# Kernel tuning notes

Measured on AMD Instinct MI355X. Metric: run time of the kernel, lower is better.

Reference implementation:

```python
import jax, jax.numpy as jnp
import numpy as np

NUM_HEADS = 8
SIGMA = 1.0
LAMBDA_INIT = 0.1
GAMMA_INIT = 0.001


def _pos_encoding(H, W, d_model):
    # 2D sinusoidal encoding: first half encodes x (width), second half y (height)
    d = d_model // 2
    div = jnp.exp(jnp.arange(0, d, 2, dtype=jnp.float32) * (-np.log(10000.0) / d))
    xs = jnp.arange(W, dtype=jnp.float32)[:, None] * div  # (W, d//2)
    ys = jnp.arange(H, dtype=jnp.float32)[:, None] * div  # (H, d//2)
    pe_x = jnp.stack([jnp.sin(xs), jnp.cos(xs)], axis=-1).reshape(W, d)
    pe_y = jnp.stack([jnp.sin(ys), jnp.cos(ys)], axis=-1).reshape(H, d)
    pe = jnp.concatenate([
        jnp.broadcast_to(pe_x[None, :, :], (H, W, d)),
        jnp.broadcast_to(pe_y[:, None, :], (H, W, d)),
    ], axis=-1)
    return pe  # (H, W, d_model)


def _distance_map(H, W, sigma):
    # exp(-euclidean_dist / sigma) between all flattened pixel positions
    yy, xx = jnp.meshgrid(jnp.arange(H, dtype=jnp.float32), jnp.arange(W, dtype=jnp.float32), indexing='ij')
    coords = jnp.stack([yy.reshape(-1), xx.reshape(-1)], axis=-1)  # (HW, 2)
    d2 = jnp.sum((coords[:, None, :] - coords[None, :, :]) ** 2, axis=-1)
    return jnp.exp(-jnp.sqrt(d2) / sigma)  # (HW, HW)


def _conv1x1(x, w, b):
    # 1x1 conv == channel matmul; x: (B,C,H,W), w: (O,C), b: (O,)
    return jnp.einsum('bchw,oc->bohw', x, w) + b[None, :, None, None]


def setup_inputs() -> dict:
    key = jax.random.key(0)
    ks = jax.random.split(key, 9)
    B, C, H, W = 2, 256, 48, 48
    d_model = 256
    inp = {
        'x': jax.random.normal(ks[0], (B, C, H, W), dtype=jnp.float32),
        'Wq': jax.random.normal(ks[1], (d_model, C), dtype=jnp.float32) * 0.01,
        'bq': jnp.zeros((d_model,), dtype=jnp.float32),
        'Wk': jax.random.normal(ks[2], (d_model, C), dtype=jnp.float32) * 0.01,
        'bk': jnp.zeros((d_model,), dtype=jnp.float32),
        'Wv': jax.random.normal(ks[3], (d_model, C), dtype=jnp.float32) * 0.01,
        'bv': jnp.zeros((d_model,), dtype=jnp.float32),
        'Wo': jax.random.normal(ks[4], (C, d_model), dtype=jnp.float32) * 0.01,
        'bo': jnp.zeros((C,), dtype=jnp.float32),
        'lambda_dist': jnp.float32(LAMBDA_INIT),
        'gamma': jnp.float32(GAMMA_INIT),
    }
    return inp


def reference(x, Wq, bq, Wk, bk, Wv, bv, Wo, bo, lambda_dist, gamma):
    B, C, H, W = x.shape
    d_model = Wq.shape[0]
    d_k = d_model // NUM_HEADS
    pe = _pos_encoding(H, W, d_model).transpose(2, 0, 1)[None]  # (1, d_model, H, W)
    dm = _distance_map(H, W, SIGMA)                              # (HW, HW)

    q = _conv1x1(x, Wq, bq) + pe
    k = _conv1x1(x, Wk, bk) + pe
    v = _conv1x1(x, Wv, bv)

    def heads(t):
        return t.reshape(B, NUM_HEADS, d_k, H * W).transpose(0, 1, 3, 2)  # (B,h,HW,d_k)

    Q, K, V = heads(q), heads(k), heads(v)
    scores = jnp.einsum('bhnd,bhmd->bhnm', Q, K) / jnp.sqrt(jnp.float32(d_k))
    scores = scores + (lambda_dist * dm)[None, None]  # 'exp' distance prior bias
    attn = jax.nn.softmax(scores, axis=-1)
    out = jnp.einsum('bhnm,bhmd->bhnd', attn, V)
    out = out.transpose(0, 1, 3, 2).reshape(B, d_model, H, W)
    fused = gamma * out  # simple weighted fusion, single (self) branch
    return x + _conv1x1(fused, Wo, bo)
```

## Files before the change

### kernel.cpp

```cpp
#include <hip/hip_runtime.h>

#define HW 2304
#define SW 48
#define DMODEL 256
#define NHEADS 8
#define DK 32
#define BATCH 2

typedef unsigned short u16;
typedef __attribute__((ext_vector_type(8))) short short8;
typedef __attribute__((ext_vector_type(4))) float f32x4;

__device__ __forceinline__ float bf2f(u16 v) {
  union { unsigned int u; float f; } c; c.u = ((unsigned int)v) << 16; return c.f;
}
__device__ __forceinline__ float lo2f(unsigned int u) {
  union { unsigned int u; float f; } c; c.u = u << 16; return c.f;
}
__device__ __forceinline__ float hi2f(unsigned int u) {
  union { unsigned int u; float f; } c; c.u = u & 0xffff0000u; return c.f;
}
__device__ __forceinline__ u16 f2bf(float f) {
  union { unsigned int u; float f; } c; c.f = f;
  unsigned int u = c.u;
  unsigned int r = (u + 0x7FFFu + ((u >> 16) & 1u)) >> 16;
  return (u16)r;
}
__device__ __forceinline__ int div48(int n) { return (n * 87382) >> 22; }
__device__ __forceinline__ int swz(int row, int k) {
  return ((row >> 4) << 12) + ((k >> 3) << 7) + ((row & 15) << 3) + (k & 7);
}

__global__ __launch_bounds__(256) void prep_kernel(
    const float* __restrict__ x,
    const float* __restrict__ Wq, const float* __restrict__ Wk,
    const float* __restrict__ Wv, const float* __restrict__ Wo,
    const float* __restrict__ lam_p,
    u16* __restrict__ xt, u16* __restrict__ Wb, u16* __restrict__ et) {
  int bid = blockIdx.x;
  int t = threadIdx.x;
  if (bid < 288) {
    int b = bid / 144, r = bid % 144;
    int c0 = (r / 36) * 64, n0 = (r % 36) * 64;
    __shared__ u16 sh[64][72];
#pragma unroll
    for (int p = 0; p < 4; ++p) {
      int row = (t >> 4) + p * 16;
      int col4 = (t & 15) * 4;
      float4 v = *(const float4*)(x + (size_t)(b * DMODEL + c0 + row) * HW +
                                  n0 + col4);
      sh[col4 + 0][row] = f2bf(v.x);
      sh[col4 + 1][row] = f2bf(v.y);
      sh[col4 + 2][row] = f2bf(v.z);
      sh[col4 + 3][row] = f2bf(v.w);
    }
    __syncthreads();
    u16* xtb = xt + (size_t)b * HW * DMODEL;
#pragma unroll
    for (int q = 0; q < 2; ++q) {
      int nrow = t >> 2;
      int c8 = (t & 3) * 8 + q * 32;
      *(uint4*)(xtb + swz(n0 + nrow, c0 + c8)) = *(const uint4*)&sh[nrow][c8];
    }
  } else if (bid < 544) {
    int idx = (bid - 288) * 1024 + t * 4;
    int which = idx >> 16, off = idx & 65535;
    int m = off >> 8, k = off & 255;
    const float* src = (which == 0) ? Wq : (which == 1) ? Wk
                       : (which == 2) ? Wv : Wo;
    float4 v = *(const float4*)(src + off);
    ushort4 ov;
    ov.x = f2bf(v.x); ov.y = f2bf(v.y); ov.z = f2bf(v.z); ov.w = f2bf(v.w);
    *(ushort4*)(Wb + which * 65536 + swz(m, k)) = ov;
  } else {
    int id = (bid - 544) * 256 + t;
    int flat = id * 8;
    int tile = flat >> 8;
    int within = flat & 255;
    int tm = tile / 144, tq = tile - tm * 144;
    int m = tm * 16 + (within >> 4);
    int q = tq * 16 + (within & 15);
    int ym = div48(m), xm = m - ym * SW;
    int yq = div48(q), xq = q - yq * SW;
    float lam = lam_p[0];
    float dy = (float)(yq - ym);
    float dy2 = dy * dy;
    u16 o[8];
#pragma unroll
    for (int j = 0; j < 8; ++j) {
      float dx = (float)(xq + j - xm);
      o[j] = f2bf(lam * __expf(-sqrtf(dy2 + dx * dx)));
    }
    *(uint4*)(et + flat) = *(const uint4*)o;
  }
}

__global__ __launch_bounds__(256) void qkv_kernel(
    const u16* __restrict__ Wb, const u16* __restrict__ xt,
    const float* __restrict__ bq, const float* __restrict__ bk,
    const float* __restrict__ bv,
    u16* __restrict__ qt, u16* __restrict__ ktb, u16* __restrict__ vb) {
  int t = threadIdx.x;
  int w = t >> 6, lane = t & 63, lo = lane & 15, quad = lane >> 4;
  int n0 = blockIdx.x * 64;
  int mb = blockIdx.y, b = blockIdx.z;
  int which = mb >> 2;
  int mrel0 = (mb & 3) * 64;
  const u16* A = Wb + which * 65536 + ((mrel0 + w * 16) >> 4) * 4096 + lo * 8;
  const float* bias = (which == 0) ? bq : (which == 1) ? bk : bv;
  const u16* Bx = xt + (size_t)b * HW * DMODEL + lo * 8;

  f32x4 acc[4] = {{0.f, 0.f, 0.f, 0.f}, {0.f, 0.f, 0.f, 0.f},
                  {0.f, 0.f, 0.f, 0.f}, {0.f, 0.f, 0.f, 0.f}};
#pragma unroll
  for (int k0 = 0; k0 < DMODEL; k0 += 32) {
    int kblk = ((k0 >> 3) + quad) << 7;
    short8 af = *(const short8*)(A + kblk);
#pragma unroll
    for (int nt = 0; nt < 4; ++nt) {
      short8 bf_ = *(const short8*)(Bx + ((n0 + nt * 16) >> 4) * 4096 + kblk);
      acc[nt] = __builtin_amdgcn_mfma_f32_16x16x32_bf16(af, bf_, acc[nt], 0, 0, 0);
    }
  }

  int mbase = mrel0 + w * 16 + quad * 4;
  if (which == 2) {
#pragma unroll
    for (int reg = 0; reg < 4; ++reg) {
      int mrel = mbase + reg;
      float bi = bias[mrel];
      u16* dst = vb + (size_t)(b * DMODEL + mrel) * HW + n0 + lo;
#pragma unroll
      for (int nt = 0; nt < 4; ++nt) dst[nt * 16] = f2bf(acc[nt][reg] + bi);
    }
  } else {
    float sc = (which == 0) ? 0.17677669529663687f : 1.0f;
    int h = mbase >> 5, d0 = mbase & 31;
    u16* base = ((which == 0) ? qt : ktb) + (size_t)(b * NHEADS + h) * HW * DK;
    float bi[4], dv[4];
    bool usecos[4], usey[4];
#pragma unroll
    for (int reg = 0; reg < 4; ++reg) {
      int mrel = mbase + reg;
      bi[reg] = bias[mrel];
      int oo = mrel & 127;
      dv[reg] = expf(-0.07195578415606394f * (float)(oo & ~1));
      usecos[reg] = (oo & 1);
      usey[reg] = (mrel >= 128);
    }
#pragma unroll
    for (int nt = 0; nt < 4; ++nt) {
      int n = n0 + nt * 16 + lo;
      int yy = div48(n), xx = n - yy * SW;
      ushort4 ov;
      float vals[4];
#pragma unroll
      for (int reg = 0; reg < 4; ++reg) {
        float tv = (usey[reg] ? (float)yy : (float)xx) * dv[reg];
        float pe = usecos[reg] ? cosf(tv) : sinf(tv);
        vals[reg] = (acc[nt][reg] + bi[reg] + pe) * sc;
      }
      ov.x = f2bf(vals[0]); ov.y = f2bf(vals[1]);
      ov.z = f2bf(vals[2]); ov.w = f2bf(vals[3]);
      *(ushort4*)(base + (size_t)n * DK + d0) = ov;
    }
  }
}

__global__ __launch_bounds__(256) void attn_kernel(
    const u16* __restrict__ qt, const u16* __restrict__ ktb,
    const u16* __restrict__ vb, const u16* __restrict__ et,
    u16* __restrict__ po_o, float* __restrict__ po_l) {
  int t = threadIdx.x;
  int w = t >> 6;
  int lane = t & 63;
  int lo = lane & 15, quad = lane >> 4;
  int n0 = blockIdx.x * 64;
  int h = blockIdx.y >> 2, kh = blockIdx.y & 3;
  int b = blockIdx.z;

  __shared__ u16 Ks[64 * 40];
  __shared__ u16 Vs[32 * 72];
  __shared__ u16 Ps[4 * 16 * 72];

  const u16* qtg = qt + (size_t)(b * NHEADS + h) * HW * DK;
  const u16* ktg = ktb + (size_t)(b * NHEADS + h) * HW * DK;
  const u16* vbg = vb + (size_t)(b * DMODEL + h * DK) * HW;

  short8 qf = *(const short8*)(qtg + (size_t)(n0 + w * 16 + lo) * DK + quad * 8);

  int tq = (n0 >> 4) + w;
  const u16* etw = et + (size_t)tq * 256 + lo * 16 + quad * 4;

  f32x4 o0 = {0.f, 0.f, 0.f, 0.f}, o1 = {0.f, 0.f, 0.f, 0.f};
  float lsum[4] = {0.f, 0.f, 0.f, 0.f};
  u16* psw = Ps + w * 16 * 72;

  for (int kt = kh * 9; kt < kh * 9 + 9; ++kt) {
    int m0 = kt * 64;
    __syncthreads();
    {
      int row = t >> 2, c8 = (t & 3) * 8;
      *(uint4*)&Ks[row * 40 + c8] =
          *(const uint4*)(ktg + (size_t)(m0 + row) * DK + c8);
      int dd = t >> 3, mo = (t & 7) * 8;
      *(uint4*)&Vs[dd * 72 + mo] =
          *(const uint4*)(vbg + (size_t)dd * HW + m0 + mo);
    }
    __syncthreads();

    uint2 ebv[4];
#pragma unroll
    for (int t4 = 0; t4 < 4; ++t4)
      ebv[t4] = *(const uint2*)(etw + (size_t)((m0 >> 4) + t4) * 36864);

    f32x4 s[4];
#pragma unroll
    for (int t4 = 0; t4 < 4; ++t4) {
      short8 kf = *(const short8*)&Ks[(t4 * 16 + lo) * 40 + quad * 8];
      f32x4 z = {0.f, 0.f, 0.f, 0.f};
      s[t4] = __builtin_amdgcn_mfma_f32_16x16x32_bf16(qf, kf, z, 0, 0, 0);
    }
#pragma unroll
    for (int t4 = 0; t4 < 4; ++t4) {
      float p0 = __expf(s[t4][0] + lo2f(ebv[t4].x));
      float p1 = __expf(s[t4][1] + hi2f(ebv[t4].x));
      float p2 = __expf(s[t4][2] + lo2f(ebv[t4].y));
      float p3 = __expf(s[t4][3] + hi2f(ebv[t4].y));
      lsum[0] += p0; lsum[1] += p1; lsum[2] += p2; lsum[3] += p3;
      psw[(quad * 4 + 0) * 72 + t4 * 16 + lo] = f2bf(p0);
      psw[(quad * 4 + 1) * 72 + t4 * 16 + lo] = f2bf(p1);
      psw[(quad * 4 + 2) * 72 + t4 * 16 + lo] = f2bf(p2);
      psw[(quad * 4 + 3) * 72 + t4 * 16 + lo] = f2bf(p3);
    }
#pragma unroll
    for (int ks = 0; ks < 2; ++ks) {
      short8 af = *(const short8*)&psw[lo * 72 + ks * 32 + quad * 8];
      short8 v0 = *(const short8*)&Vs[lo * 72 + ks * 32 + quad * 8];
      o0 = __builtin_amdgcn_mfma_f32_16x16x32_bf16(af, v0, o0, 0, 0, 0);
      short8 v1 = *(const short8*)&Vs[(16 + lo) * 72 + ks * 32 + quad * 8];
      o1 = __builtin_amdgcn_mfma_f32_16x16x32_bf16(af, v1, o1, 0, 0, 0);
    }
  }

#pragma unroll
  for (int d = 1; d < 16; d <<= 1) {
#pragma unroll
    for (int reg = 0; reg < 4; ++reg) lsum[reg] += __shfl_xor(lsum[reg], d);
  }

  int slot = (b * NHEADS + h) * 36 + blockIdx.x;
  u16* pw = po_o + (size_t)(kh * 576 + slot) * 2048 + w * 512;
  ushort4 s0, s1;
  s0.x = f2bf(o0[0]); s0.y = f2bf(o0[1]); s0.z = f2bf(o0[2]); s0.w = f2bf(o0[3]);
  s1.x = f2bf(o1[0]); s1.y = f2bf(o1[1]); s1.z = f2bf(o1[2]); s1.w = f2bf(o1[3]);
  *(ushort4*)(pw + lane * 4) = s0;
  *(ushort4*)(pw + 256 + lane * 4) = s1;
  if (lo == 0) {
    float4 lv = make_float4(lsum[0], lsum[1], lsum[2], lsum[3]);
    *(float4*)(po_l + (size_t)(kh * 576 + slot) * 64 + w * 16 + quad * 4) = lv;
  }
}

__global__ __launch_bounds__(256) void reduce_kernel(
    const u16* __restrict__ po_o, const float* __restrict__ po_l,
    u16* __restrict__ aot) {
  int t = threadIdx.x;
  int w = t >> 6, lane = t & 63, lo = lane & 15, quad = lane >> 4;
  int qt_ = blockIdx.x, h = blockIdx.y, b = blockIdx.z;
  int slot = (b * NHEADS + h) * 36 + qt_;

  float s0[4] = {0.f, 0.f, 0.f, 0.f}, s1[4] = {0.f, 0.f, 0.f, 0.f};
  float lt[4] = {0.f, 0.f, 0.f, 0.f};
#pragma unroll
  for (int kh = 0; kh < 4; ++kh) {
    const u16* p = po_o + (size_t)(kh * 576 + slot) * 2048 + w * 512;
    ushort4 a0 = *(const ushort4*)(p + lane * 4);
    ushort4 a1 = *(const ushort4*)(p + 256 + lane * 4);
    s0[0] += bf2f(a0.x); s0[1] += bf2f(a0.y);
    s0[2] += bf2f(a0.z); s0[3] += bf2f(a0.w);
    s1[0] += bf2f(a1.x); s1[1] += bf2f(a1.y);
    s1[2] += bf2f(a1.z); s1[3] += bf2f(a1.w);
    float4 lv = *(const float4*)(po_l + (size_t)(kh * 576 + slot) * 64 +
                                 w * 16 + quad * 4);
    lt[0] += lv.x; lt[1] += lv.y; lt[2] += lv.z; lt[3] += lv.w;
  }

  u16* aog = aot + (size_t)b * HW * DMODEL;
#pragma unroll
  for (int reg = 0; reg < 4; ++reg) {
    float inv = 1.0f / lt[reg];
    int n = qt_ * 64 + w * 16 + quad * 4 + reg;
    aog[swz(n, h * DK + lo)] = f2bf(s0[reg] * inv);
    aog[swz(n, h * DK + 16 + lo)] = f2bf(s1[reg] * inv);
  }
}

__global__ __launch_bounds__(256) void out_kernel(
    const float* __restrict__ x, const u16* __restrict__ Wob,
    const float* __restrict__ bo, const float* __restrict__ gp,
    const u16* __restrict__ aot, float* __restrict__ out) {
  int t = threadIdx.x;
  int w = t >> 6, lane = t & 63, lo = lane & 15, quad = lane >> 4;
  int n0 = blockIdx.x * 64;
  int c0 = blockIdx.y * 64;
  int b = blockIdx.z;
  float gamma = gp[0];
  const u16* A = Wob + ((c0 + w * 16) >> 4) * 4096 + lo * 8;
  const u16* Ba = aot + (size_t)b * HW * DMODEL + lo * 8;

  f32x4 acc[4] = {{0.f, 0.f, 0.f, 0.f}, {0.f, 0.f, 0.f, 0.f},
                  {0.f, 0.f, 0.f, 0.f}, {0.f, 0.f, 0.f, 0.f}};
#pragma unroll
  for (int k0 = 0; k0 < DMODEL; k0 += 32) {
    int kblk = ((k0 >> 3) + quad) << 7;
    short8 af = *(const short8*)(A + kblk);
#pragma unroll
    for (int nt = 0; nt < 4; ++nt) {
      short8 bf_ = *(const short8*)(Ba + ((n0 + nt * 16) >> 4) * 4096 + kblk);
      acc[nt] = __builtin_amdgcn_mfma_f32_16x16x32_bf16(af, bf_, acc[nt], 0, 0, 0);
    }
  }

#pragma unroll
  for (int reg = 0; reg < 4; ++reg) {
    int c = c0 + w * 16 + quad * 4 + reg;
    float bi = bo[c];
    const float* xs = x + (size_t)(b * DMODEL + c) * HW + n0 + lo;
    float* os = out + (size_t)(b * DMODEL + c) * HW + n0 + lo;
#pragma unroll
    for (int nt = 0; nt < 4; ++nt)
      os[nt * 16] = xs[nt * 16] + gamma * acc[nt][reg] + bi;
  }
}

extern "C" void kernel_launch(void* const* d_in, const int* in_sizes, int n_in,
                              void* d_out, int out_size, void* d_ws,
                              size_t ws_size, hipStream_t stream) {
  const float* x   = (const float*)d_in[0];
  const float* Wq  = (const float*)d_in[1];
  const float* bq  = (const float*)d_in[2];
  const float* Wk  = (const float*)d_in[3];
  const float* bk  = (const float*)d_in[4];
  const float* Wv  = (const float*)d_in[5];
  const float* bv  = (const float*)d_in[6];
  const float* Wo  = (const float*)d_in[7];
  const float* bo  = (const float*)d_in[8];
  const float* lam = (const float*)d_in[9];
  const float* gam = (const float*)d_in[10];

  char* wsb = (char*)d_ws;
  u16* Wb  = (u16*)(wsb + 36864);
  u16* xt  = (u16*)(wsb + 561152);
  u16* aot = xt;
  u16* qt  = (u16*)(wsb + 2920448);
  u16* ktb = (u16*)(wsb + 5279744);
  u16* vb  = (u16*)(wsb + 7639040);
  u16* et  = (u16*)(wsb + 9998336);
  u16* po_o = (u16*)(wsb + 20615168);
  float* po_l = (float*)(wsb + 30052352);
  float* out = (float*)d_out;

  prep_kernel<<<dim3(3136), 256, 0, stream>>>(x, Wq, Wk, Wv, Wo, lam,
                                              xt, Wb, et);
  qkv_kernel<<<dim3(36, 12, BATCH), 256, 0, stream>>>(Wb, xt, bq, bk, bv,
                                                      qt, ktb, vb);
  attn_kernel<<<dim3(36, 32, BATCH), 256, 0, stream>>>(qt, ktb, vb, et,
                                                       po_o, po_l);
  reduce_kernel<<<dim3(36, 8, BATCH), 256, 0, stream>>>(po_o, po_l, aot);
  out_kernel<<<dim3(36, 4, BATCH), 256, 0, stream>>>(x, Wb + 3 * 65536, bo, gam,
                                                     aot, out);
}
```

Baseline: 136.9 us.

## Compute transposed scores so P stays in registers, removing LDS round-trip

The attention kernel now computes S^T = K·Q^T with K rows permuted at load time, so each lane's MFMA output maps directly onto the B-operand fragment of the P·V MFMA. This removes the per-tile shared-memory buffer for P, its scattered 16-bit stores and reloads, and the per-row shuffle reduction of the row sums. The bias table must use a matching, differently tiled layout, and the output and row-sum layouts change, so the reduce kernel is updated to match. It relies on the prep code having produced the new bias layout; if it has not, results will be wrong.

```diff
diff --git a/kernel.cpp b/kernel.cpp
--- a/kernel.cpp
+++ b/kernel.cpp
@@ -181,7 +181,6 @@
 
   __shared__ u16 Ks[64 * 40];
   __shared__ u16 Vs[32 * 72];
-  __shared__ u16 Ps[4 * 16 * 72];
 
   const u16* qtg = qt + (size_t)(b * NHEADS + h) * HW * DK;
   const u16* ktg = ktb + (size_t)(b * NHEADS + h) * HW * DK;
@@ -189,65 +188,64 @@
 
   short8 qf = *(const short8*)(qtg + (size_t)(n0 + w * 16 + lo) * DK + quad * 8);
 
+  int srow = t >> 2;
+  int sks = srow >> 5, srr = srow & 31;
+  int sv = (srr < 16) ? (8 * (srr >> 2) + (srr & 3))
+                      : (8 * ((srr - 16) >> 2) + 4 + ((srr - 16) & 3));
+  int skey = sks * 32 + sv;
+  int sc8 = (t & 3) * 8;
+
   int tq = (n0 >> 4) + w;
-  const u16* etw = et + (size_t)tq * 256 + lo * 16 + quad * 4;
+  const u16* etw = et + (size_t)tq * 144 * 256 + lo * 16 + (quad & 1) * 8;
+  int qh = quad >> 1;
 
   f32x4 o0 = {0.f, 0.f, 0.f, 0.f}, o1 = {0.f, 0.f, 0.f, 0.f};
-  float lsum[4] = {0.f, 0.f, 0.f, 0.f};
-  u16* psw = Ps + w * 16 * 72;
+  float lsum = 0.f;
 
   for (int kt = kh * 9; kt < kh * 9 + 9; ++kt) {
     int m0 = kt * 64;
     __syncthreads();
     {
-      int row = t >> 2, c8 = (t & 3) * 8;
-      *(uint4*)&Ks[row * 40 + c8] =
-          *(const uint4*)(ktg + (size_t)(m0 + row) * DK + c8);
+      *(uint4*)&Ks[srow * 40 + sc8] =
+          *(const uint4*)(ktg + (size_t)(m0 + skey) * DK + sc8);
       int dd = t >> 3, mo = (t & 7) * 8;
       *(uint4*)&Vs[dd * 72 + mo] =
           *(const uint4*)(vbg + (size_t)dd * HW + m0 + mo);
     }
     __syncthreads();
 
-    uint2 ebv[4];
-#pragma unroll
-    for (int t4 = 0; t4 < 4; ++t4)
-      ebv[t4] = *(const uint2*)(etw + (size_t)((m0 >> 4) + t4) * 36864);
-
-    f32x4 s[4];
-#pragma unroll
-    for (int t4 = 0; t4 < 4; ++t4) {
-      short8 kf = *(const short8*)&Ks[(t4 * 16 + lo) * 40 + quad * 8];
+    uint4 eb0 = *(const uint4*)(etw + (size_t)((m0 >> 4) + 0 + qh) * 256);
+    uint4 eb1 = *(const uint4*)(etw + (size_t)((m0 >> 4) + 2 + qh) * 256);
+
+#pragma unroll
+    for (int ks = 0; ks < 2; ++ks) {
+      uint4 ebv = ks ? eb1 : eb0;
+      short8 kfA = *(const short8*)&Ks[(ks * 32 + lo) * 40 + quad * 8];
+      short8 kfB = *(const short8*)&Ks[(ks * 32 + 16 + lo) * 40 + quad * 8];
       f32x4 z = {0.f, 0.f, 0.f, 0.f};
-      s[t4] = __builtin_amdgcn_mfma_f32_16x16x32_bf16(qf, kf, z, 0, 0, 0);
-    }
-#pragma unroll
-    for (int t4 = 0; t4 < 4; ++t4) {
-      float p0 = __expf(s[t4][0] + lo2f(ebv[t4].x));
-      float p1 = __expf(s[t4][1] + hi2f(ebv[t4].x));
-      float p2 = __expf(s[t4][2] + lo2f(ebv[t4].y));
-      float p3 = __expf(s[t4][3] + hi2f(ebv[t4].y));
-      lsum[0] += p0; lsum[1] += p1; lsum[2] += p2; lsum[3] += p3;
-      psw[(quad * 4 + 0) * 72 + t4 * 16 + lo] = f2bf(p0);
-      psw[(quad * 4 + 1) * 72 + t4 * 16 + lo] = f2bf(p1);
-      psw[(quad * 4 + 2) * 72 + t4 * 16 + lo] = f2bf(p2);
-      psw[(quad * 4 + 3) * 72 + t4 * 16 + lo] = f2bf(p3);
-    }
-#pragma unroll
-    for (int ks = 0; ks < 2; ++ks) {
-      short8 af = *(const short8*)&psw[lo * 72 + ks * 32 + quad * 8];
+      f32x4 sA = __builtin_amdgcn_mfma_f32_16x16x32_bf16(kfA, qf, z, 0, 0, 0);
+      f32x4 sB = __builtin_amdgcn_mfma_f32_16x16x32_bf16(kfB, qf, z, 0, 0, 0);
+      float p0 = __expf(sA[0] + lo2f(ebv.x));
+      float p1 = __expf(sA[1] + hi2f(ebv.x));
+      float p2 = __expf(sA[2] + lo2f(ebv.y));
+      float p3 = __expf(sA[3] + hi2f(ebv.y));
+      float p4 = __expf(sB[0] + lo2f(ebv.z));
+      float p5 = __expf(sB[1] + hi2f(ebv.z));
+      float p6 = __expf(sB[2] + lo2f(ebv.w));
+      float p7 = __expf(sB[3] + hi2f(ebv.w));
+      lsum += ((p0 + p1) + (p2 + p3)) + ((p4 + p5) + (p6 + p7));
+      u16 pk[8] = {f2bf(p0), f2bf(p1), f2bf(p2), f2bf(p3),
+                   f2bf(p4), f2bf(p5), f2bf(p6), f2bf(p7)};
+      short8 pfrag = *(const short8*)pk;
       short8 v0 = *(const short8*)&Vs[lo * 72 + ks * 32 + quad * 8];
-      o0 = __builtin_amdgcn_mfma_f32_16x16x32_bf16(af, v0, o0, 0, 0, 0);
+      o0 = __builtin_amdgcn_mfma_f32_16x16x32_bf16(v0, pfrag, o0, 0, 0, 0);
       short8 v1 = *(const short8*)&Vs[(16 + lo) * 72 + ks * 32 + quad * 8];
-      o1 = __builtin_amdgcn_mfma_f32_16x16x32_bf16(af, v1, o1, 0, 0, 0);
-    }
-  }
-
-#pragma unroll
-  for (int d = 1; d < 16; d <<= 1) {
-#pragma unroll
-    for (int reg = 0; reg < 4; ++reg) lsum[reg] += __shfl_xor(lsum[reg], d);
-  }
+      o1 = __builtin_amdgcn_mfma_f32_16x16x32_bf16(v1, pfrag, o1, 0, 0, 0);
+    }
+  }
+
+  lsum += __shfl_xor(lsum, 16);
+  lsum += __shfl_xor(lsum, 32);
 
   int slot = (b * NHEADS + h) * 36 + blockIdx.x;
   u16* pw = po_o + (size_t)(kh * 576 + slot) * 2048 + w * 512;
@@ -256,10 +254,8 @@
   s1.x = f2bf(o1[0]); s1.y = f2bf(o1[1]); s1.z = f2bf(o1[2]); s1.w = f2bf(o1[3]);
   *(ushort4*)(pw + lane * 4) = s0;
   *(ushort4*)(pw + 256 + lane * 4) = s1;
-  if (lo == 0) {
-    float4 lv = make_float4(lsum[0], lsum[1], lsum[2], lsum[3]);
-    *(float4*)(po_l + (size_t)(kh * 576 + slot) * 64 + w * 16 + quad * 4) = lv;
-  }
+  if (quad == 0)
+    po_l[(size_t)(kh * 576 + slot) * 64 + w * 16 + lo] = lsum;
 }
 
 __global__ __launch_bounds__(256) void reduce_kernel(
@@ -271,7 +267,7 @@
   int slot = (b * NHEADS + h) * 36 + qt_;
 
   float s0[4] = {0.f, 0.f, 0.f, 0.f}, s1[4] = {0.f, 0.f, 0.f, 0.f};
-  float lt[4] = {0.f, 0.f, 0.f, 0.f};
+  float lt = 0.f;
 #pragma unroll
   for (int kh = 0; kh < 4; ++kh) {
     const u16* p = po_o + (size_t)(kh * 576 + slot) * 2048 + w * 512;
@@ -281,19 +277,19 @@
     s0[2] += bf2f(a0.z); s0[3] += bf2f(a0.w);
     s1[0] += bf2f(a1.x); s1[1] += bf2f(a1.y);
     s1[2] += bf2f(a1.z); s1[3] += bf2f(a1.w);
-    float4 lv = *(const float4*)(po_l + (size_t)(kh * 576 + slot) * 64 +
-                                 w * 16 + quad * 4);
-    lt[0] += lv.x; lt[1] += lv.y; lt[2] += lv.z; lt[3] += lv.w;
-  }
-
+    lt += po_l[(size_t)(kh * 576 + slot) * 64 + w * 16 + lo];
+  }
+  float inv = 1.0f / lt;
+
+  int n = qt_ * 64 + w * 16 + lo;
   u16* aog = aot + (size_t)b * HW * DMODEL;
-#pragma unroll
-  for (int reg = 0; reg < 4; ++reg) {
-    float inv = 1.0f / lt[reg];
-    int n = qt_ * 64 + w * 16 + quad * 4 + reg;
-    aog[swz(n, h * DK + lo)] = f2bf(s0[reg] * inv);
-    aog[swz(n, h * DK + 16 + lo)] = f2bf(s1[reg] * inv);
-  }
+  ushort4 w0, w1;
+  w0.x = f2bf(s0[0] * inv); w0.y = f2bf(s0[1] * inv);
+  w0.z = f2bf(s0[2] * inv); w0.w = f2bf(s0[3] * inv);
+  w1.x = f2bf(s1[0] * inv); w1.y = f2bf(s1[1] * inv);
+  w1.z = f2bf(s1[2] * inv); w1.w = f2bf(s1[3] * inv);
+  *(ushort4*)&aog[swz(n, h * DK + quad * 4)] = w0;
+  *(ushort4*)&aog[swz(n, h * DK + 16 + quad * 4)] = w1;
 }
 
 __global__ __launch_bounds__(256) void out_kernel(
```

Result: no change. 134.7 us (-1.6%).
